# Kernel tuning notes

Measured on AMD Instinct MI355X. Metric: run time of the kernel, lower is better.

## Reference

```python
import jax, jax.numpy as jnp
import numpy as np

B, N, D, H, K = 8, 128, 256, 128, 8

def setup_inputs() -> dict:
    key = jax.random.key(0)
    ks = jax.random.split(key, 6)
    E = jax.random.normal(ks[0], (B, N, D), dtype=jnp.float32)
    # kaiming_uniform-like init for linear weights
    lim1 = np.sqrt(6.0 / (2 * D))
    W1 = jax.random.uniform(ks[1], (H, 2 * D), minval=-lim1, maxval=lim1, dtype=jnp.float32)
    b1 = jnp.zeros((H,), dtype=jnp.float32)
    lim2 = np.sqrt(6.0 / H)
    W2 = jax.random.uniform(ks[2], (D, H), minval=-lim2, maxval=lim2, dtype=jnp.float32)
    b2 = jnp.zeros((D,), dtype=jnp.float32)
    q = jax.random.normal(ks[3], (K, D), dtype=jnp.float32) * (1.0 / D ** 0.5)
    return {"E": E, "W1": W1, "b1": b1, "W2": W2, "b2": b2, "q": q}

def reference(E, W1, b1, W2, b2, q):
    # phi(cat(Ei,Ej)) == relu(E_i @ W1a^T + E_j @ W1b^T + b1) @ W2^T + b2
    # Split first linear's weight to avoid materializing the [B,N,N,2D] concat.
    W1a, W1b = W1[:, :D], W1[:, D:]          # each [H, D]
    Ai = jnp.einsum('bnd,hd->bnh', E, W1a)   # [B,N,H] (row half)
    Aj = jnp.einsum('bnd,hd->bnh', E, W1b)   # [B,N,H] (col half)
    hidden = jax.nn.relu(Ai[:, :, None, :] + Aj[:, None, :, :] + b1)  # [B,N,N,H]
    # dropout is identity at inference
    # Fuse second linear with query dot: (hidden @ W2^T + b2) . q_h
    #   = hidden @ (W2^T q_h) + b2.q_h
    Wq = jnp.einsum('dh,kd->hk', W2, q)      # [H, K]
    bq = jnp.einsum('d,kd->k', b2, q)        # [K]
    logits = jnp.einsum('bijh,hk->bijh'[:0] or 'bijh,hk->bijk', hidden, Wq) + bq  # [B,N,N,K]
    M = jax.nn.sigmoid(logits).transpose(0, 3, 1, 2)  # [B,K,N,N]
    eye = jnp.eye(N, dtype=M.dtype)[None, None]
    return M * (1.0 - eye)
```

## Files before the change

### kernel.cpp

```cpp
#include <hip/hip_runtime.h>

#define PB 8
#define PN 128
#define PD 256
#define PH 128
#define PK 8
#define D2 (2*PD)

__global__ __launch_bounds__(256) void k0_prep(
        const float* __restrict__ W1, const float* __restrict__ W2,
        const float* __restrict__ b2, const float* __restrict__ q,
        float4* __restrict__ W1t4, float* __restrict__ Wq, float* __restrict__ bq)
{
    const int blk = blockIdx.x, t = threadIdx.x;
    if (blk < 64) {
        __shared__ float sm[32][33];
        const int h0 = (blk >> 4) * 32;
        const int d0 = (blk & 15) * 32;
        const int tx = t & 31, ty = t >> 5;
        #pragma unroll
        for (int r = 0; r < 4; ++r)
            sm[ty + 8 * r][tx] = W1[(h0 + ty + 8 * r) * D2 + d0 + tx];
        __syncthreads();
        const int hl = t & 31, dql = t >> 5;
        float4 w = make_float4(sm[hl][dql * 4 + 0], sm[hl][dql * 4 + 1],
                               sm[hl][dql * 4 + 2], sm[hl][dql * 4 + 3]);
        W1t4[((d0 >> 2) + dql) * PH + h0 + hl] = w;
    } else {
        __shared__ float qs[PD];
        __shared__ float red[256];
        const int k = blk - 64;
        qs[t] = q[k * PD + t];
        __syncthreads();
        if (t < PH) {
            float acc = 0.f;
            #pragma unroll 4
            for (int d = 0; d < PD; ++d)
                acc = fmaf(W2[d * PH + t], qs[d], acc);
            Wq[t * PK + k] = acc;
        }
        red[t] = b2[t] * qs[t];
        __syncthreads();
        for (int st = 128; st > 0; st >>= 1) {
            if (t < st) red[t] += red[t + st];
            __syncthreads();
        }
        if (t == 0) bq[k] = red[0];
    }
}

__global__ __launch_bounds__(256, 2) void k1_proj(
        const float* __restrict__ E, const float* __restrict__ b1,
        const float4* __restrict__ W1t4,
        float* __restrict__ Ai, float* __restrict__ Ajt)
{
    __shared__ float4 psum[PH];
    const int blk = blockIdx.x, t = threadIdx.x;
    const int b    = blk >> 6;
    const int part = (blk >> 5) & 1;
    const int rg   = blk & 31;
    const int h    = t & (PH - 1);
    const int s    = t >> 7;
    const int n0   = rg * 4;

    const int ebase = __builtin_amdgcn_readfirstlane((b * PN + n0) * PD + s * 128);
    const float* e0 = E + ebase;
    const float* e1 = e0 + PD;
    const float* e2 = e1 + PD;
    const float* e3 = e2 + PD;
    const float4* wp = W1t4 + (part * 64 + s * 32) * PH + h;

    float a0 = 0.f, a1 = 0.f, a2 = 0.f, a3 = 0.f;
    #pragma unroll 8
    for (int dq = 0; dq < 32; ++dq) {
        const float4 w  = wp[dq * PH];
        const float4 p0 = *reinterpret_cast<const float4*>(e0 + dq * 4);
        const float4 p1 = *reinterpret_cast<const float4*>(e1 + dq * 4);
        const float4 p2 = *reinterpret_cast<const float4*>(e2 + dq * 4);
        const float4 p3 = *reinterpret_cast<const float4*>(e3 + dq * 4);
        a0 = fmaf(w.x, p0.x, a0); a0 = fmaf(w.y, p0.y, a0);
        a0 = fmaf(w.z, p0.z, a0); a0 = fmaf(w.w, p0.w, a0);
        a1 = fmaf(w.x, p1.x, a1); a1 = fmaf(w.y, p1.y, a1);
        a1 = fmaf(w.z, p1.z, a1); a1 = fmaf(w.w, p1.w, a1);
        a2 = fmaf(w.x, p2.x, a2); a2 = fmaf(w.y, p2.y, a2);
        a2 = fmaf(w.z, p2.z, a2); a2 = fmaf(w.w, p2.w, a2);
        a3 = fmaf(w.x, p3.x, a3); a3 = fmaf(w.y, p3.y, a3);
        a3 = fmaf(w.z, p3.z, a3); a3 = fmaf(w.w, p3.w, a3);
    }

    if (s == 1)
        psum[h] = make_float4(a0, a1, a2, a3);
    __syncthreads();
    if (s == 0) {
        const float4 p = psum[h];
        a0 += p.x; a1 += p.y; a2 += p.z; a3 += p.w;
        if (part == 0) {
            const float bb = b1[h];
            Ai[(b * PN + n0 + 0) * PH + h] = a0 + bb;
            Ai[(b * PN + n0 + 1) * PH + h] = a1 + bb;
            Ai[(b * PN + n0 + 2) * PH + h] = a2 + bb;
            Ai[(b * PN + n0 + 3) * PH + h] = a3 + bb;
        } else {
            *reinterpret_cast<float4*>(&Ajt[(b * PH + h) * PN + n0]) =
                make_float4(a0, a1, a2, a3);
        }
    }
}

__global__ __launch_bounds__(256, 2) void k2_score(
        const float* __restrict__ Ai, const float* __restrict__ Ajt,
        const float4* __restrict__ Wq4, const float* __restrict__ bq,
        float* __restrict__ out)
{
    const int blk = blockIdx.x, t = threadIdx.x;
    const int b  = blk >> 6;
    const int ip = blk & 63;
    const int il = t >> 7;
    const int i  = ip * 2 + il;
    const int j  = t & (PN - 1);

    const int aib = __builtin_amdgcn_readfirstlane((b * PN + i) * PH);
    const float* ai = Ai + aib;
    const float* aj = Ajt + b * PH * PN + j;

    float acc[PK];
    #pragma unroll
    for (int k = 0; k < PK; ++k) acc[k] = bq[k];

    #pragma unroll 8
    for (int hh = 0; hh < PH; ++hh) {
        const float a = ai[hh];
        const float g = aj[hh * PN];
        const float v = fmaxf(a + g, 0.f);
        const float4 wA = Wq4[hh * 2];
        const float4 wB = Wq4[hh * 2 + 1];
        acc[0] = fmaf(v, wA.x, acc[0]); acc[1] = fmaf(v, wA.y, acc[1]);
        acc[2] = fmaf(v, wA.z, acc[2]); acc[3] = fmaf(v, wA.w, acc[3]);
        acc[4] = fmaf(v, wB.x, acc[4]); acc[5] = fmaf(v, wB.y, acc[5]);
        acc[6] = fmaf(v, wB.z, acc[6]); acc[7] = fmaf(v, wB.w, acc[7]);
    }

    #pragma unroll
    for (int k = 0; k < PK; ++k) {
        float sg = 1.f / (1.f + __expf(-acc[k]));
        if (j == i) sg = 0.f;
        out[((b * PK + k) * PN + i) * PN + j] = sg;
    }
}

extern "C" void kernel_launch(void* const* d_in, const int* in_sizes, int n_in,
                              void* d_out, int out_size, void* d_ws, size_t ws_size,
                              hipStream_t stream) {
    const float* E  = (const float*)d_in[0];
    const float* W1 = (const float*)d_in[1];
    const float* b1 = (const float*)d_in[2];
    const float* W2 = (const float*)d_in[3];
    const float* b2 = (const float*)d_in[4];
    const float* q  = (const float*)d_in[5];

    float*  Ai   = (float*)d_ws;
    float*  Ajt  = Ai + PB * PN * PH;
    float4* W1t4 = (float4*)(Ajt + PB * PH * PN);
    float*  Wq   = (float*)(W1t4 + 128 * PH);
    float*  bq   = Wq + PH * PK;

    k0_prep<<<72,  256, 0, stream>>>(W1, W2, b2, q, W1t4, Wq, bq);
    k1_proj<<<512, 256, 0, stream>>>(E, b1, W1t4, Ai, Ajt);
    k2_score<<<512, 256, 0, stream>>>(Ai, Ajt, (const float4*)Wq, bq, (float*)d_out);
}
```

Baseline: 102.6 us.

## Fuse three kernels into one cooperative launch with grid syncs

Merges the prep, projection and scoring kernels into one cooperative kernel that uses grid-wide syncs between phases, and falls back to the three separate launches if the cooperative launch fails. The aim is to remove the gaps and launch overhead between kernels. In exchange it adds two grid barriers and requires all 512 blocks to be co-resident. Blocks 72 and up sit idle during the prep phase.

```diff
diff --git a/kernel.cpp b/kernel.cpp
--- a/kernel.cpp
+++ b/kernel.cpp
@@ -1,4 +1,7 @@
 #include <hip/hip_runtime.h>
+#include <hip/hip_cooperative_groups.h>
+
+namespace cg = cooperative_groups;
 
 #define PB 8
 #define PN 128
@@ -7,29 +10,28 @@
 #define PK 8
 #define D2 (2*PD)
 
-__global__ __launch_bounds__(256) void k0_prep(
+
+__device__ __forceinline__ void prep_phase(
         const float* __restrict__ W1, const float* __restrict__ W2,
         const float* __restrict__ b2, const float* __restrict__ q,
-        float4* __restrict__ W1t4, float* __restrict__ Wq, float* __restrict__ bq)
-{
-    const int blk = blockIdx.x, t = threadIdx.x;
+        float4* __restrict__ W1t4, float* __restrict__ Wq, float* __restrict__ bq,
+        int blk, int t, float* sm , float* red )
+{
     if (blk < 64) {
-        __shared__ float sm[32][33];
         const int h0 = (blk >> 4) * 32;
         const int d0 = (blk & 15) * 32;
         const int tx = t & 31, ty = t >> 5;
         #pragma unroll
         for (int r = 0; r < 4; ++r)
-            sm[ty + 8 * r][tx] = W1[(h0 + ty + 8 * r) * D2 + d0 + tx];
+            sm[(ty + 8 * r) * 33 + tx] = W1[(h0 + ty + 8 * r) * D2 + d0 + tx];
         __syncthreads();
         const int hl = t & 31, dql = t >> 5;
-        float4 w = make_float4(sm[hl][dql * 4 + 0], sm[hl][dql * 4 + 1],
-                               sm[hl][dql * 4 + 2], sm[hl][dql * 4 + 3]);
+        float4 w = make_float4(sm[hl * 33 + dql * 4 + 0], sm[hl * 33 + dql * 4 + 1],
+                               sm[hl * 33 + dql * 4 + 2], sm[hl * 33 + dql * 4 + 3]);
         W1t4[((d0 >> 2) + dql) * PH + h0 + hl] = w;
-    } else {
-        __shared__ float qs[PD];
-        __shared__ float red[256];
+    } else if (blk < 72) {
         const int k = blk - 64;
+        float* qs = sm;
         qs[t] = q[k * PD + t];
         __syncthreads();
         if (t < PH) {
@@ -49,13 +51,12 @@
     }
 }
 
-__global__ __launch_bounds__(256, 2) void k1_proj(
+__device__ __forceinline__ void proj_phase(
         const float* __restrict__ E, const float* __restrict__ b1,
         const float4* __restrict__ W1t4,
-        float* __restrict__ Ai, float* __restrict__ Ajt)
-{
-    __shared__ float4 psum[PH];
-    const int blk = blockIdx.x, t = threadIdx.x;
+        float* __restrict__ Ai, float* __restrict__ Ajt,
+        int blk, int t, float4* psum )
+{
     const int b    = blk >> 6;
     const int part = (blk >> 5) & 1;
     const int rg   = blk & 31;
@@ -107,12 +108,11 @@
     }
 }
 
-__global__ __launch_bounds__(256, 2) void k2_score(
+__device__ __forceinline__ void score_phase(
         const float* __restrict__ Ai, const float* __restrict__ Ajt,
         const float4* __restrict__ Wq4, const float* __restrict__ bq,
-        float* __restrict__ out)
-{
-    const int blk = blockIdx.x, t = threadIdx.x;
+        float* __restrict__ out, int blk, int t)
+{
     const int b  = blk >> 6;
     const int ip = blk & 63;
     const int il = t >> 7;
@@ -148,6 +148,53 @@
     }
 }
 
+__global__ __launch_bounds__(256, 2) void fused_all(
+        const float* __restrict__ E,  const float* __restrict__ W1,
+        const float* __restrict__ b1, const float* __restrict__ W2,
+        const float* __restrict__ b2, const float* __restrict__ q,
+        float4* __restrict__ W1t4, float* __restrict__ Wq, float* __restrict__ bq,
+        float* __restrict__ Ai, float* __restrict__ Ajt, float* __restrict__ out)
+{
+    __shared__ float  sm[32 * 33];
+    __shared__ float  red[256];
+    __shared__ float4 psum[PH];
+
+    const int blk = blockIdx.x, t = threadIdx.x;
+
+    prep_phase(W1, W2, b2, q, W1t4, Wq, bq, blk, t, sm, red);
+    cg::this_grid().sync();
+    proj_phase(E, b1, W1t4, Ai, Ajt, blk, t, psum);
+    cg::this_grid().sync();
+    score_phase(Ai, Ajt, (const float4*)Wq, bq, out, blk, t);
+}
+
+__global__ __launch_bounds__(256) void k0_prep(
+        const float* __restrict__ W1, const float* __restrict__ W2,
+        const float* __restrict__ b2, const float* __restrict__ q,
+        float4* __restrict__ W1t4, float* __restrict__ Wq, float* __restrict__ bq)
+{
+    __shared__ float sm[32 * 33];
+    __shared__ float red[256];
+    prep_phase(W1, W2, b2, q, W1t4, Wq, bq, blockIdx.x, threadIdx.x, sm, red);
+}
+
+__global__ __launch_bounds__(256, 2) void k1_proj(
+        const float* __restrict__ E, const float* __restrict__ b1,
+        const float4* __restrict__ W1t4,
+        float* __restrict__ Ai, float* __restrict__ Ajt)
+{
+    __shared__ float4 psum[PH];
+    proj_phase(E, b1, W1t4, Ai, Ajt, blockIdx.x, threadIdx.x, psum);
+}
+
+__global__ __launch_bounds__(256, 2) void k2_score(
+        const float* __restrict__ Ai, const float* __restrict__ Ajt,
+        const float4* __restrict__ Wq4, const float* __restrict__ bq,
+        float* __restrict__ out)
+{
+    score_phase(Ai, Ajt, Wq4, bq, out, blockIdx.x, threadIdx.x);
+}
+
 extern "C" void kernel_launch(void* const* d_in, const int* in_sizes, int n_in,
                               void* d_out, int out_size, void* d_ws, size_t ws_size,
                               hipStream_t stream) {
@@ -163,8 +210,18 @@
     float4* W1t4 = (float4*)(Ajt + PB * PH * PN);
     float*  Wq   = (float*)(W1t4 + 128 * PH);
     float*  bq   = Wq + PH * PK;
-
-    k0_prep<<<72,  256, 0, stream>>>(W1, W2, b2, q, W1t4, Wq, bq);
-    k1_proj<<<512, 256, 0, stream>>>(E, b1, W1t4, Ai, Ajt);
-    k2_score<<<512, 256, 0, stream>>>(Ai, Ajt, (const float4*)Wq, bq, (float*)d_out);
-}
+    float*  out  = (float*)d_out;
+
+    void* args[] = { (void*)&E, (void*)&W1, (void*)&b1, (void*)&W2,
+                     (void*)&b2, (void*)&q,  (void*)&W1t4, (void*)&Wq,
+                     (void*)&bq, (void*)&Ai, (void*)&Ajt, (void*)&out };
+
+    hipError_t err = hipLaunchCooperativeKernel(
+        (const void*)fused_all, dim3(512), dim3(256), args, 0, stream);
+    if (err != hipSuccess) {
+        (void)hipGetLastError();
+        k0_prep<<<72,  256, 0, stream>>>(W1, W2, b2, q, W1t4, Wq, bq);
+        k1_proj<<<512, 256, 0, stream>>>(E, b1, W1t4, Ai, Ajt);
+        k2_score<<<512, 256, 0, stream>>>(Ai, Ajt, (const float4*)Wq, bq, out);
+    }
+}
```

Measured after the change: 233.5 us. +127.6%, slower.

## Fuse W1 transpose prep into projection kernel via swizzled LDS staging

Applied to the files above, without the earlier changes.

Removes the separate W1 transpose pass and its global scratch buffer. The projection blocks now load W1 row-major directly into XOR-swizzled shared memory in two 32-quad chunks and read it transposed from there, while the Wq/bq prep runs as extra blocks of the same launch. This drops one kernel launch and one global round trip. In exchange each block uses 64KB of LDS, which limits occupancy, and block count and per-block work are restructured (8 rows per block, no split-d reduction).

```diff
diff --git a/kernel.cpp b/kernel.cpp
--- a/kernel.cpp
+++ b/kernel.cpp
@@ -7,29 +7,82 @@
 #define PK 8
 #define D2 (2*PD)
 
-__global__ __launch_bounds__(256) void k0_prep(
-        const float* __restrict__ W1, const float* __restrict__ W2,
+__global__ __launch_bounds__(256) void kA_proj(
+        const float* __restrict__ E,  const float* __restrict__ W1,
+        const float* __restrict__ b1, const float* __restrict__ W2,
         const float* __restrict__ b2, const float* __restrict__ q,
-        float4* __restrict__ W1t4, float* __restrict__ Wq, float* __restrict__ bq)
+        float* __restrict__ Ai, float* __restrict__ Ajt,
+        float* __restrict__ Wq, float* __restrict__ bq)
 {
+    __shared__ float4 wlds[32 * 128];
     const int blk = blockIdx.x, t = threadIdx.x;
-    if (blk < 64) {
-        __shared__ float sm[32][33];
-        const int h0 = (blk >> 4) * 32;
-        const int d0 = (blk & 15) * 32;
-        const int tx = t & 31, ty = t >> 5;
+
+    if (blk < 256) {
+        const int b    = blk >> 5;
+        const int part = (blk >> 4) & 1;
+        const int rg   = blk & 15;
+        const int h    = t & (PH - 1);
+        const int s    = t >> 7;
+        const int n0   = rg * 8 + s * 4;
+
+        const int ebase = __builtin_amdgcn_readfirstlane((b * PN + n0) * PD);
+        const float* e0 = E + ebase;
+        const float* e1 = e0 + PD;
+        const float* e2 = e1 + PD;
+        const float* e3 = e2 + PD;
+
+        const int dql = t & 31;
+        const int h2  = t >> 5;
+
+        float a0 = 0.f, a1 = 0.f, a2 = 0.f, a3 = 0.f;
+
         #pragma unroll
-        for (int r = 0; r < 4; ++r)
-            sm[ty + 8 * r][tx] = W1[(h0 + ty + 8 * r) * D2 + d0 + tx];
-        __syncthreads();
-        const int hl = t & 31, dql = t >> 5;
-        float4 w = make_float4(sm[hl][dql * 4 + 0], sm[hl][dql * 4 + 1],
-                               sm[hl][dql * 4 + 2], sm[hl][dql * 4 + 3]);
-        W1t4[((d0 >> 2) + dql) * PH + h0 + hl] = w;
+        for (int p = 0; p < 2; ++p) {
+            const int dqb = p * 32;
+            const float* wsrc = W1 + part * PD + (dqb + dql) * 4;
+            float4* wdst = &wlds[dql * 128];
+            #pragma unroll
+            for (int r = 0; r < 16; ++r) {
+                const int hh = h2 * 16 + r;
+                wdst[hh ^ (dql & 7)] =
+                    *reinterpret_cast<const float4*>(wsrc + hh * D2);
+            }
+            __syncthreads();
+            #pragma unroll 4
+            for (int dq = 0; dq < 32; ++dq) {
+                const float4 w = wlds[dq * 128 + (h ^ (dq & 7))];
+                const int dd = (dqb + dq) * 4;
+                const float4 p0 = *reinterpret_cast<const float4*>(e0 + dd);
+                const float4 p1 = *reinterpret_cast<const float4*>(e1 + dd);
+                const float4 p2 = *reinterpret_cast<const float4*>(e2 + dd);
+                const float4 p3 = *reinterpret_cast<const float4*>(e3 + dd);
+                a0 = fmaf(w.x, p0.x, a0); a0 = fmaf(w.y, p0.y, a0);
+                a0 = fmaf(w.z, p0.z, a0); a0 = fmaf(w.w, p0.w, a0);
+                a1 = fmaf(w.x, p1.x, a1); a1 = fmaf(w.y, p1.y, a1);
+                a1 = fmaf(w.z, p1.z, a1); a1 = fmaf(w.w, p1.w, a1);
+                a2 = fmaf(w.x, p2.x, a2); a2 = fmaf(w.y, p2.y, a2);
+                a2 = fmaf(w.z, p2.z, a2); a2 = fmaf(w.w, p2.w, a2);
+                a3 = fmaf(w.x, p3.x, a3); a3 = fmaf(w.y, p3.y, a3);
+                a3 = fmaf(w.z, p3.z, a3); a3 = fmaf(w.w, p3.w, a3);
+            }
+            __syncthreads();
+        }
+
+        if (part == 0) {
+            const float bb = b1[h];
+            Ai[(b * PN + n0 + 0) * PH + h] = a0 + bb;
+            Ai[(b * PN + n0 + 1) * PH + h] = a1 + bb;
+            Ai[(b * PN + n0 + 2) * PH + h] = a2 + bb;
+            Ai[(b * PN + n0 + 3) * PH + h] = a3 + bb;
+        } else {
+            *reinterpret_cast<float4*>(&Ajt[(b * PH + h) * PN + n0]) =
+                make_float4(a0, a1, a2, a3);
+        }
     } else {
-        __shared__ float qs[PD];
-        __shared__ float red[256];
-        const int k = blk - 64;
+        float* smf = reinterpret_cast<float*>(wlds);
+        float* qs  = smf;
+        float* red = smf + PD;
+        const int k = blk - 256;
         qs[t] = q[k * PD + t];
         __syncthreads();
         if (t < PH) {
@@ -49,65 +102,7 @@
     }
 }
 
-__global__ __launch_bounds__(256, 2) void k1_proj(
-        const float* __restrict__ E, const float* __restrict__ b1,
-        const float4* __restrict__ W1t4,
-        float* __restrict__ Ai, float* __restrict__ Ajt)
-{
-    __shared__ float4 psum[PH];
-    const int blk = blockIdx.x, t = threadIdx.x;
-    const int b    = blk >> 6;
-    const int part = (blk >> 5) & 1;
-    const int rg   = blk & 31;
-    const int h    = t & (PH - 1);
-    const int s    = t >> 7;
-    const int n0   = rg * 4;
-
-    const int ebase = __builtin_amdgcn_readfirstlane((b * PN + n0) * PD + s * 128);
-    const float* e0 = E + ebase;
-    const float* e1 = e0 + PD;
-    const float* e2 = e1 + PD;
-    const float* e3 = e2 + PD;
-    const float4* wp = W1t4 + (part * 64 + s * 32) * PH + h;
-
-    float a0 = 0.f, a1 = 0.f, a2 = 0.f, a3 = 0.f;
-    #pragma unroll 8
-    for (int dq = 0; dq < 32; ++dq) {
-        const float4 w  = wp[dq * PH];
-        const float4 p0 = *reinterpret_cast<const float4*>(e0 + dq * 4);
-        const float4 p1 = *reinterpret_cast<const float4*>(e1 + dq * 4);
-        const float4 p2 = *reinterpret_cast<const float4*>(e2 + dq * 4);
-        const float4 p3 = *reinterpret_cast<const float4*>(e3 + dq * 4);
-        a0 = fmaf(w.x, p0.x, a0); a0 = fmaf(w.y, p0.y, a0);
-        a0 = fmaf(w.z, p0.z, a0); a0 = fmaf(w.w, p0.w, a0);
-        a1 = fmaf(w.x, p1.x, a1); a1 = fmaf(w.y, p1.y, a1);
-        a1 = fmaf(w.z, p1.z, a1); a1 = fmaf(w.w, p1.w, a1);
-        a2 = fmaf(w.x, p2.x, a2); a2 = fmaf(w.y, p2.y, a2);
-        a2 = fmaf(w.z, p2.z, a2); a2 = fmaf(w.w, p2.w, a2);
-        a3 = fmaf(w.x, p3.x, a3); a3 = fmaf(w.y, p3.y, a3);
-        a3 = fmaf(w.z, p3.z, a3); a3 = fmaf(w.w, p3.w, a3);
-    }
-
-    if (s == 1)
-        psum[h] = make_float4(a0, a1, a2, a3);
-    __syncthreads();
-    if (s == 0) {
-        const float4 p = psum[h];
-        a0 += p.x; a1 += p.y; a2 += p.z; a3 += p.w;
-        if (part == 0) {
-            const float bb = b1[h];
-            Ai[(b * PN + n0 + 0) * PH + h] = a0 + bb;
-            Ai[(b * PN + n0 + 1) * PH + h] = a1 + bb;
-            Ai[(b * PN + n0 + 2) * PH + h] = a2 + bb;
-            Ai[(b * PN + n0 + 3) * PH + h] = a3 + bb;
-        } else {
-            *reinterpret_cast<float4*>(&Ajt[(b * PH + h) * PN + n0]) =
-                make_float4(a0, a1, a2, a3);
-        }
-    }
-}
-
-__global__ __launch_bounds__(256, 2) void k2_score(
+__global__ __launch_bounds__(256, 2) void kB_score(
         const float* __restrict__ Ai, const float* __restrict__ Ajt,
         const float4* __restrict__ Wq4, const float* __restrict__ bq,
         float* __restrict__ out)
@@ -158,13 +153,11 @@
     const float* b2 = (const float*)d_in[4];
     const float* q  = (const float*)d_in[5];
 
-    float*  Ai   = (float*)d_ws;
-    float*  Ajt  = Ai + PB * PN * PH;
-    float4* W1t4 = (float4*)(Ajt + PB * PH * PN);
-    float*  Wq   = (float*)(W1t4 + 128 * PH);
-    float*  bq   = Wq + PH * PK;
+    float* Ai  = (float*)d_ws;
+    float* Ajt = Ai + PB * PN * PH;
+    float* Wq  = Ajt + PB * PH * PN;
+    float* bq  = Wq + PH * PK;
 
-    k0_prep<<<72,  256, 0, stream>>>(W1, W2, b2, q, W1t4, Wq, bq);
-    k1_proj<<<512, 256, 0, stream>>>(E, b1, W1t4, Ai, Ajt);
-    k2_score<<<512, 256, 0, stream>>>(Ai, Ajt, (const float4*)Wq, bq, (float*)d_out);
+    kA_proj<<<264, 256, 0, stream>>>(E, W1, b1, W2, b2, q, Ai, Ajt, Wq, bq);
+    kB_score<<<512, 256, 0, stream>>>(Ai, Ajt, (const float4*)Wq, bq, (float*)d_out);
 }
```

Result: faster. 93.87 us (-8.5%).
